# Performance work log

Hardware: AMD Instinct MI355X
Metric: run time of the kernel (lower is better)

Reference implementation:

```python
import jax, jax.numpy as jnp
import numpy as np

B, H, W, D, DFF = 32, 40, 40, 128, 2048
S = H * W  # 1600
BN_EPS = 1e-5


def setup_inputs() -> dict:
    key = jax.random.key(0)
    ks = jax.random.split(key, 8)
    se = jax.random.normal(ks[2], (H, W, H, W), dtype=jnp.float32)
    se = se + jnp.transpose(se, (2, 3, 0, 1))  # symmetric init as in torch code
    wscale = 0.02
    return {
        "tgt": jax.random.normal(ks[0], (B, H, W, D), dtype=jnp.float32),
        "memory": jax.random.normal(ks[1], (B, H, W, D), dtype=jnp.float32),
        "score_embed": se,
        "w1": jax.random.normal(ks[3], (D, D), dtype=jnp.float32) * wscale,
        "b1": jnp.zeros((D,), jnp.float32),
        "g1": jnp.ones((2 * S,), jnp.float32),
        "be1": jnp.zeros((2 * S,), jnp.float32),
        "w2": jax.random.normal(ks[4], (DFF, 2 * S), dtype=jnp.float32) * wscale,
        "b2": jnp.zeros((DFF,), jnp.float32),
        "g2": jnp.ones((DFF,), jnp.float32),
        "be2": jnp.zeros((DFF,), jnp.float32),
        "w3": jax.random.normal(ks[5], (1, DFF), dtype=jnp.float32) * wscale,
        "b3": jnp.zeros((1,), jnp.float32),
        "g3": jnp.ones((1,), jnp.float32),
        "be3": jnp.zeros((1,), jnp.float32),
    }


def _bn_eval(x, gamma, beta):
    # BatchNorm eval mode with running_mean=0, running_var=1 (as initialized)
    return x * (gamma / jnp.sqrt(1.0 + BN_EPS)) + beta


def _l2norm(x):
    # F.normalize(p=2, dim=-1) with eps=1e-12
    return x / jnp.maximum(jnp.linalg.norm(x, axis=-1, keepdims=True), 1e-12)


def reference(tgt, memory, score_embed, w1, b1, g1, be1, w2, b2, g2, be2, w3, b3, g3, be3):
    b, h, w, d = tgt.shape
    s = h * w
    q = _l2norm(tgt.reshape(b, s, d) @ w1.T + b1)   # [B,S,D]
    k = _l2norm(memory.reshape(b, s, d) @ w1.T + b1)
    gate = jax.nn.sigmoid(score_embed.reshape(s, s))  # [S,S]
    attn = jnp.einsum("bsd,btd->bst", q, k) * gate    # [B,S,S]
    m1 = attn.max(axis=1)  # max over dim 1 -> [B,S]
    m2 = attn.max(axis=2)  # max over dim 2 -> [B,S]
    x = jnp.concatenate([m1, m2], axis=1)  # [B,2S]
    x = _bn_eval(x, g1, be1)
    x = x @ w2.T + b2        # [B,DFF]
    x = jax.nn.relu(_bn_eval(x, g2, be2))
    x = x @ w3.T + b3        # [B,1]
    x = _bn_eval(x, g3, be3)
    return x.squeeze(-1)     # [B]
```

## Files before the change

kernel.cpp:

```cpp
#include <hip/hip_runtime.h>
#include <hip/hip_bf16.h>

#define BB 32
#define SS 1600
#define DD 128
#define DFFN 2048
#define S2N 3200
#define RS 136

typedef __attribute__((ext_vector_type(8))) short short8;
typedef __attribute__((ext_vector_type(4))) float floatx4;
typedef unsigned int u32;
typedef unsigned short u16;

__device__ __forceinline__ u32 encf(float f) {
  u32 u = __float_as_uint(f);
  return (u & 0x80000000u) ? ~u : (u | 0x80000000u);
}
__device__ __forceinline__ float decf(u32 e) {
  u32 u = (e & 0x80000000u) ? (e & 0x7fffffffu) : ~e;
  return __uint_as_float(u);
}
__device__ __forceinline__ u16 f2b(float x) {
  u32 u = __float_as_uint(x);
  return (u16)((u + 0x7FFFu + ((u >> 16) & 1u)) >> 16);
}
__device__ __forceinline__ u32 packb2(float lo, float hi) {
  return (u32)f2b(lo) | ((u32)f2b(hi) << 16);
}
__device__ __forceinline__ float sigm(float x) { return 1.f / (1.f + __expf(-x)); }

__global__ __launch_bounds__(256) void k_prep(const float* __restrict__ tgt,
                                              const float* __restrict__ memin,
                                              const float* __restrict__ w1,
                                              const float* __restrict__ b1,
                                              const float* __restrict__ se,
                                              u16* __restrict__ qb, u16* __restrict__ kb,
                                              u16* __restrict__ gT2,
                                              u32* __restrict__ m1u, u32* __restrict__ m2u) {
  __shared__ u16 sA[128 * RS];
  __shared__ u16 sB[128 * RS];
  __shared__ float sq[128];
  int tid = threadIdx.x;
  int lane = tid & 63, wv = tid >> 6;
  int wr = wv >> 1, wc = wv & 1;
  int l15 = lane & 15, lg = lane >> 4;

  if (blockIdx.x >= 800) {
    int bid = blockIdx.x - 800;
    int ii = bid * 256 + tid;
    if (ii < BB * SS) {
      m1u[ii] = 0u;
      m2u[ii] = 0u;
    }
    int r2 = bid >> 2, mi = bid & 3;
    int sy = r2 / 13, tx = r2 - sy * 13;
    int s0 = min(sy * 128, SS - 128);
    int t0 = min(tx * 128, SS - 128);
    int srow = s0 + wr * 64 + mi * 16 + lg * 4;
    u16* tb = gT2 + (size_t)r2 * 16384 + wv * 4096 + lane * 8;
    for (int ni = 0; ni < 4; ++ni) {
      int tcol = t0 + wc * 64 + ni * 16 + l15;
      const float* sp = se + (size_t)srow * SS + tcol;
      ushort4 o;
      o.x = f2b(sigm(sp[0]));
      o.y = f2b(sigm(sp[SS]));
      o.z = f2b(sigm(sp[2 * SS]));
      o.w = f2b(sigm(sp[3 * SS]));
      *(ushort4*)(tb + (mi * 2 + (ni >> 1)) * 512 + (ni & 1) * 4) = o;
    }
    return;
  }

  long row0 = (long)blockIdx.x * 128;
  const float* src;
  u16* dst;
  if (row0 < (long)BB * SS) { src = tgt + row0 * DD; dst = qb + row0 * DD; }
  else { src = memin + (row0 - (long)BB * SS) * DD; dst = kb + (row0 - (long)BB * SS) * DD; }

  for (int p = 0; p < 16; ++p) {
    int r = p * 8 + (tid >> 5);
    int c4 = (tid & 31) * 4;
    float4 v = *(const float4*)(src + r * DD + c4);
    *(u32*)&sA[r * RS + c4] = packb2(v.x, v.y);
    *(u32*)&sA[r * RS + c4 + 2] = packb2(v.z, v.w);
    float4 w = *(const float4*)(w1 + r * DD + c4);
    *(u32*)&sB[r * RS + c4] = packb2(w.x, w.y);
    *(u32*)&sB[r * RS + c4 + 2] = packb2(w.z, w.w);
  }
  if (tid < 128) sq[tid] = 0.f;
  __syncthreads();

  floatx4 acc[4][4];
  for (int mi = 0; mi < 4; ++mi)
    for (int ni = 0; ni < 4; ++ni) acc[mi][ni] = (floatx4){0.f, 0.f, 0.f, 0.f};

  for (int kc = 0; kc < 4; ++kc) {
    int k0 = kc * 32 + lg * 8;
    short8 af[4], bfr[4];
    for (int mi = 0; mi < 4; ++mi) af[mi] = *(const short8*)&sA[(wr * 64 + mi * 16 + l15) * RS + k0];
    for (int ni = 0; ni < 4; ++ni) bfr[ni] = *(const short8*)&sB[(wc * 64 + ni * 16 + l15) * RS + k0];
    for (int mi = 0; mi < 4; ++mi)
      for (int ni = 0; ni < 4; ++ni)
        acc[mi][ni] = __builtin_amdgcn_mfma_f32_16x16x32_bf16(af[mi], bfr[ni], acc[mi][ni], 0, 0, 0);
  }

  float bvals[4];
  for (int ni = 0; ni < 4; ++ni) bvals[ni] = b1[wc * 64 + ni * 16 + l15];
  for (int mi = 0; mi < 4; ++mi)
    for (int r = 0; r < 4; ++r) {
      float s = 0.f;
      for (int ni = 0; ni < 4; ++ni) {
        float v = acc[mi][ni][r] + bvals[ni];
        acc[mi][ni][r] = v;
        s += v * v;
      }
      s += __shfl_xor(s, 1); s += __shfl_xor(s, 2);
      s += __shfl_xor(s, 4); s += __shfl_xor(s, 8);
      if (l15 == 0) atomicAdd(&sq[wr * 64 + mi * 16 + lg * 4 + r], s);
    }
  __syncthreads();

  for (int mi = 0; mi < 4; ++mi)
    for (int r = 0; r < 4; ++r) {
      int row = wr * 64 + mi * 16 + lg * 4 + r;
      float scale = 1.f / fmaxf(sqrtf(sq[row]), 1e-12f);
      for (int ni = 0; ni < 4; ++ni)
        sA[row * RS + wc * 64 + ni * 16 + l15] = f2b(acc[mi][ni][r] * scale);
    }
  __syncthreads();
  for (int p = 0; p < 8; ++p) {
    int r = p * 16 + (tid >> 4);
    int c8 = (tid & 15) * 8;
    *(uint4*)(dst + r * DD + c8) = *(const uint4*)&sA[r * RS + c8];
  }
}

__global__ __launch_bounds__(256, 4) void k_attn(const u16* __restrict__ qb,
                                                 const u16* __restrict__ kb,
                                                 const u16* __restrict__ gT2,
                                                 u32* __restrict__ m1u, u32* __restrict__ m2u) {
  __shared__ u16 sK[128 * RS];
  __shared__ float scmax[2][128];
  __shared__ float srmax[2][128];
  int tid = threadIdx.x;
  int n = blockIdx.x;
  int m = n >> 3;
  int r2 = m >> 2;
  int b = (n & 7) * 4 + (m & 3);
  int sy = r2 / 13, tx = r2 - sy * 13;
  int s0 = min(sy * 128, SS - 128);
  int t0 = min(tx * 128, SS - 128);
  int lane = tid & 63, wv = tid >> 6;
  int wr = wv >> 1, wc = wv & 1;
  int l15 = lane & 15, lg = lane >> 4;
  const size_t base = (size_t)b * SS * DD;
  const u16* qp = qb + base + (size_t)(s0 + wr * 64 + l15) * DD + lg * 8;

  {
    int rr0 = tid >> 4;
    int c8 = (tid & 15) * 8;
    const u16* kp = kb + base + (size_t)(t0 + rr0) * DD + c8;
    u16* sp = &sK[rr0 * RS + c8];
    for (int p = 0; p < 8; ++p)
      *(uint4*)(sp + p * 16 * RS) = *(const uint4*)(kp + (size_t)p * 16 * DD);
  }
  short8 qsA[4], qsB[4];
  for (int mi = 0; mi < 4; ++mi) qsA[mi] = *(const short8*)(qp + mi * 16 * DD);
  __syncthreads();

  floatx4 acc[4][4];
  for (int mi = 0; mi < 4; ++mi)
    for (int ni = 0; ni < 4; ++ni) acc[mi][ni] = (floatx4){0.f, 0.f, 0.f, 0.f};

#define QKSTEP(KC, CUR, NXT, PRE)                                                     \
  {                                                                                   \
    if (PRE)                                                                          \
      for (int mi = 0; mi < 4; ++mi)                                                  \
        NXT[mi] = *(const short8*)(qp + mi * 16 * DD + ((KC) + 1) * 32);              \
    int k0 = (KC)*32 + lg * 8;                                                        \
    short8 bfr[4];                                                                    \
    for (int ni = 0; ni < 4; ++ni)                                                    \
      bfr[ni] = *(const short8*)&sK[(wc * 64 + ni * 16 + l15) * RS + k0];             \
    for (int mi = 0; mi < 4; ++mi)                                                    \
      for (int ni = 0; ni < 4; ++ni)                                                  \
        acc[mi][ni] = __builtin_amdgcn_mfma_f32_16x16x32_bf16(CUR[mi], bfr[ni],       \
                                                              acc[mi][ni], 0, 0, 0);  \
  }
  QKSTEP(0, qsA, qsB, 1)
  QKSTEP(1, qsB, qsA, 1)
  QKSTEP(2, qsA, qsB, 1)
  QKSTEP(3, qsB, qsA, 0)
#undef QKSTEP

  uint4 g4[8];
  {
    const u16* gbase = gT2 + (size_t)r2 * 16384 + wv * 4096 + lane * 8;
    for (int p = 0; p < 8; ++p) g4[p] = *(const uint4*)(gbase + p * 512);
  }

  float rmax[4][4];
  for (int mi = 0; mi < 4; ++mi)
    for (int r = 0; r < 4; ++r) rmax[mi][r] = -1e30f;
  float cmax[4];
  for (int ni = 0; ni < 4; ++ni) cmax[ni] = -1e30f;

  for (int mi = 0; mi < 4; ++mi)
    for (int ni = 0; ni < 4; ++ni) {
      uint4 pg = g4[mi * 2 + (ni >> 1)];
      u32 lo = (ni & 1) ? pg.z : pg.x;
      u32 hi = (ni & 1) ? pg.w : pg.y;
      float v0 = acc[mi][ni][0] * __uint_as_float(lo << 16);
      float v1 = acc[mi][ni][1] * __uint_as_float(lo & 0xffff0000u);
      float v2 = acc[mi][ni][2] * __uint_as_float(hi << 16);
      float v3 = acc[mi][ni][3] * __uint_as_float(hi & 0xffff0000u);
      rmax[mi][0] = fmaxf(rmax[mi][0], v0);
      rmax[mi][1] = fmaxf(rmax[mi][1], v1);
      rmax[mi][2] = fmaxf(rmax[mi][2], v2);
      rmax[mi][3] = fmaxf(rmax[mi][3], v3);
      cmax[ni] = fmaxf(cmax[ni], fmaxf(fmaxf(v0, v1), fmaxf(v2, v3)));
    }

  for (int ni = 0; ni < 4; ++ni) {
    cmax[ni] = fmaxf(cmax[ni], __shfl_xor(cmax[ni], 16));
    cmax[ni] = fmaxf(cmax[ni], __shfl_xor(cmax[ni], 32));
  }
  if (lane < 16)
    for (int ni = 0; ni < 4; ++ni) scmax[wr][wc * 64 + ni * 16 + lane] = cmax[ni];

  for (int mi = 0; mi < 4; ++mi)
    for (int r = 0; r < 4; ++r) {
      float v = rmax[mi][r];
      v = fmaxf(v, __shfl_xor(v, 1));
      v = fmaxf(v, __shfl_xor(v, 2));
      v = fmaxf(v, __shfl_xor(v, 4));
      v = fmaxf(v, __shfl_xor(v, 8));
      if (l15 == 0) srmax[wc][wr * 64 + mi * 16 + lg * 4 + r] = v;
    }
  __syncthreads();

  if (tid < 128) {
    float v = fmaxf(scmax[0][tid], scmax[1][tid]);
    atomicMax(&m1u[b * SS + t0 + tid], encf(v));
  } else {
    int i2 = tid - 128;
    float v = fmaxf(srmax[0][i2], srmax[1][i2]);
    atomicMax(&m2u[b * SS + s0 + i2], encf(v));
  }
}

__global__ __launch_bounds__(256) void k_gemm2(const u32* __restrict__ m1u,
                                               const u32* __restrict__ m2u,
                                               const float* __restrict__ g1,
                                               const float* __restrict__ be1,
                                               const float* __restrict__ w2,
                                               float* __restrict__ hacc) {
  int tid = threadIdx.x;
  int lane = tid & 63, wv = tid >> 6;
  int f0 = blockIdx.x * 32 + wv * 8;
  int cs = blockIdx.y;
  int cr0 = cs * 200;
  const u32* msrc = (cs < 8) ? m1u : m2u;
  int mcol0 = cr0 - ((cs < 8) ? 0 : SS);
  int c_sub = lane & 15, bq = lane >> 4;
  const float bnc = rsqrtf(1.f + 1e-5f);
  float acc[8][8];
  for (int a = 0; a < 8; ++a)
    for (int c = 0; c < 8; ++c) acc[a][c] = 0.f;
  const float4 z4 = {0.f, 0.f, 0.f, 0.f};
  for (int it = 0; it < 4; ++it) {
    int coff = it * 64 + c_sub * 4;
    bool ok = coff < 200;
    int cg = cr0 + coff;
    float4 w4[8], x4[8];
    float4 gv = ok ? *(const float4*)(g1 + cg) : z4;
    float4 bv = ok ? *(const float4*)(be1 + cg) : z4;
    gv.x *= bnc; gv.y *= bnc; gv.z *= bnc; gv.w *= bnc;
    for (int jf = 0; jf < 8; ++jf)
      w4[jf] = ok ? *(const float4*)(w2 + (size_t)(f0 + jf) * S2N + cg) : z4;
    for (int j = 0; j < 8; ++j) {
      if (ok) {
        uint4 e = *(const uint4*)(msrc + (size_t)(bq * 8 + j) * SS + mcol0 + coff);
        x4[j].x = decf(e.x) * gv.x + bv.x;
        x4[j].y = decf(e.y) * gv.y + bv.y;
        x4[j].z = decf(e.z) * gv.z + bv.z;
        x4[j].w = decf(e.w) * gv.w + bv.w;
      } else {
        x4[j] = z4;
      }
    }
    for (int jf = 0; jf < 8; ++jf)
      for (int j = 0; j < 8; ++j) {
        float a = acc[jf][j];
        a = fmaf(w4[jf].x, x4[j].x, a);
        a = fmaf(w4[jf].y, x4[j].y, a);
        a = fmaf(w4[jf].z, x4[j].z, a);
        a = fmaf(w4[jf].w, x4[j].w, a);
        acc[jf][j] = a;
      }
  }
  for (int jf = 0; jf < 8; ++jf)
    for (int j = 0; j < 8; ++j) {
      float v = acc[jf][j];
      v += __shfl_xor(v, 1); v += __shfl_xor(v, 2);
      v += __shfl_xor(v, 4); v += __shfl_xor(v, 8);
      acc[jf][j] = v;
    }
  if ((lane & 15) == 0) {
    for (int jf = 0; jf < 8; ++jf)
      for (int j = 0; j < 8; ++j) {
        int b = bq * 8 + j;
        hacc[((size_t)cs * BB + b) * DFFN + f0 + jf] = acc[jf][j];
      }
  }
}

__global__ __launch_bounds__(512) void k_final(const float* __restrict__ hacc,
                                               const float* __restrict__ b2,
                                               const float* __restrict__ g2,
                                               const float* __restrict__ be2,
                                               const float* __restrict__ w3,
                                               const float* __restrict__ b3,
                                               const float* __restrict__ g3,
                                               const float* __restrict__ be3,
                                               float* __restrict__ out) {
  __shared__ float wsum[8];
  int b = blockIdx.x;
  int tid = threadIdx.x;
  float bnc = rsqrtf(1.f + 1e-5f);
  int f4i = tid;
  float4 s4 = *(const float4*)(b2 + f4i * 4);
  for (int cs = 0; cs < 16; ++cs) {
    float4 h = *(const float4*)(hacc + ((size_t)cs * BB + b) * DFFN + f4i * 4);
    s4.x += h.x; s4.y += h.y; s4.z += h.z; s4.w += h.w;
  }
  float4 gv = *(const float4*)(g2 + f4i * 4);
  float4 bv = *(const float4*)(be2 + f4i * 4);
  float4 w4 = *(const float4*)(w3 + f4i * 4);
  float part = 0.f;
  part += fmaxf(s4.x * (gv.x * bnc) + bv.x, 0.f) * w4.x;
  part += fmaxf(s4.y * (gv.y * bnc) + bv.y, 0.f) * w4.y;
  part += fmaxf(s4.z * (gv.z * bnc) + bv.z, 0.f) * w4.z;
  part += fmaxf(s4.w * (gv.w * bnc) + bv.w, 0.f) * w4.w;
  for (int m = 1; m < 64; m <<= 1) part += __shfl_xor(part, m);
  if ((tid & 63) == 0) wsum[tid >> 6] = part;
  __syncthreads();
  if (tid == 0) {
    float tot = b3[0];
    for (int wq = 0; wq < 8; ++wq) tot += wsum[wq];
    out[b] = tot * (g3[0] * bnc) + be3[0];
  }
}

extern "C" void kernel_launch(void* const* d_in, const int* in_sizes, int n_in,
                              void* d_out, int out_size, void* d_ws, size_t ws_size,
                              hipStream_t stream) {
  const float* tgt = (const float*)d_in[0];
  const float* memin = (const float*)d_in[1];
  const float* se = (const float*)d_in[2];
  const float* w1 = (const float*)d_in[3];
  const float* b1 = (const float*)d_in[4];
  const float* g1 = (const float*)d_in[5];
  const float* be1 = (const float*)d_in[6];
  const float* w2 = (const float*)d_in[7];
  const float* b2 = (const float*)d_in[8];
  const float* g2 = (const float*)d_in[9];
  const float* be2 = (const float*)d_in[10];
  const float* w3 = (const float*)d_in[11];
  const float* b3 = (const float*)d_in[12];
  const float* g3 = (const float*)d_in[13];
  const float* be3 = (const float*)d_in[14];
  float* out = (float*)d_out;

  char* ws = (char*)d_ws;
  const size_t OFF_GT = 0;
  const size_t OFF_QB = 5537792;
  const size_t OFF_KB = OFF_QB + 13107200;
  const size_t OFF_M1 = OFF_KB + 13107200;
  const size_t OFF_M2 = OFF_M1 + 204800;
  const size_t OFF_HA = OFF_M2 + 204800;
  const size_t NEEDED = OFF_HA + 4194304;
  if (ws_size < NEEDED) return;

  u16* gT2 = (u16*)(ws + OFF_GT);
  u16* qb = (u16*)(ws + OFF_QB);
  u16* kb = (u16*)(ws + OFF_KB);
  u32* m1u = (u32*)(ws + OFF_M1);
  u32* m2u = (u32*)(ws + OFF_M2);
  float* hacc = (float*)(ws + OFF_HA);

  k_prep<<<1476, 256, 0, stream>>>(tgt, memin, w1, b1, se, qb, kb, gT2, m1u, m2u);
  k_attn<<<5408, 256, 0, stream>>>(qb, kb, gT2, m1u, m2u);
  k_gemm2<<<dim3(64, 16), 256, 0, stream>>>(m1u, m2u, g1, be1, w2, hacc);
  k_final<<<32, 512, 0, stream>>>(hacc, b2, g2, be2, w3, b3, g3, be3, out);
}
```

Measured before the change: 135.6 us.

## Split projection prep into bf16 conversion kernel and register-fed projection GEMM

Replaces the fused prep kernel with two kernels. A streaming kernel converts tgt, memory and w1 to bf16, computes the sigmoid gate tiles and zeroes the max buffers. A separate projection kernel then reads the bf16 activations and weights straight from global memory into registers, double-buffering the A fragments, and normalizes rows in place. This removes LDS staging and the per-block re-conversion of w1, at the cost of an extra launch and an extra round trip of the bf16 activations through memory. The hacc workspace is moved to overlap the gate buffer.

```diff
diff --git a/kernel.cpp b/kernel.cpp
--- a/kernel.cpp
+++ b/kernel.cpp
@@ -30,80 +30,111 @@
 }
 __device__ __forceinline__ float sigm(float x) { return 1.f / (1.f + __expf(-x)); }
 
-__global__ __launch_bounds__(256) void k_prep(const float* __restrict__ tgt,
+__global__ __launch_bounds__(256) void k_conv(const float* __restrict__ tgt,
                                               const float* __restrict__ memin,
                                               const float* __restrict__ w1,
-                                              const float* __restrict__ b1,
                                               const float* __restrict__ se,
                                               u16* __restrict__ qb, u16* __restrict__ kb,
+                                              u16* __restrict__ w1b,
                                               u16* __restrict__ gT2,
                                               u32* __restrict__ m1u, u32* __restrict__ m2u) {
-  __shared__ u16 sA[128 * RS];
-  __shared__ u16 sB[128 * RS];
+  int tid = threadIdx.x;
+  int bid = blockIdx.x;
+  if (bid < 1600) {
+    const float4* src4;
+    uint2* dst2;
+    int cb;
+    if (bid < 800) { src4 = (const float4*)tgt; dst2 = (uint2*)qb; cb = bid; }
+    else { src4 = (const float4*)memin; dst2 = (uint2*)kb; cb = bid - 800; }
+    int base = cb * 2048 + tid;
+    float4 v[8];
+    for (int j = 0; j < 8; ++j) v[j] = src4[base + j * 256];
+    for (int j = 0; j < 8; ++j) {
+      uint2 o;
+      o.x = packb2(v[j].x, v[j].y);
+      o.y = packb2(v[j].z, v[j].w);
+      dst2[base + j * 256] = o;
+    }
+    return;
+  }
+  int gbid = bid - 1600;
+  int ii = gbid * 256 + tid;
+  if (ii < 4096) {
+    float4 w = ((const float4*)w1)[ii];
+    ushort4 o;
+    o.x = f2b(w.x); o.y = f2b(w.y); o.z = f2b(w.z); o.w = f2b(w.w);
+    ((ushort4*)w1b)[ii] = o;
+  }
+  if (ii < BB * SS) {
+    m1u[ii] = 0u;
+    m2u[ii] = 0u;
+  }
+  int lane = tid & 63, wv = tid >> 6;
+  int wr = wv >> 1, wc = wv & 1;
+  int l15 = lane & 15, lg = lane >> 4;
+  int r2 = gbid >> 2, mi = gbid & 3;
+  int sy = r2 / 13, tx = r2 - sy * 13;
+  int s0 = min(sy * 128, SS - 128);
+  int t0 = min(tx * 128, SS - 128);
+  int srow = s0 + wr * 64 + mi * 16 + lg * 4;
+  u16* tb = gT2 + (size_t)r2 * 16384 + wv * 4096 + lane * 8;
+  for (int ni = 0; ni < 4; ++ni) {
+    int tcol = t0 + wc * 64 + ni * 16 + l15;
+    const float* sp = se + (size_t)srow * SS + tcol;
+    ushort4 o;
+    o.x = f2b(sigm(sp[0]));
+    o.y = f2b(sigm(sp[SS]));
+    o.z = f2b(sigm(sp[2 * SS]));
+    o.w = f2b(sigm(sp[3 * SS]));
+    *(ushort4*)(tb + (mi * 2 + (ni >> 1)) * 512 + (ni & 1) * 4) = o;
+  }
+}
+
+__global__ __launch_bounds__(256, 3) void k_proj(u16* __restrict__ qb, u16* __restrict__ kb,
+                                                 const u16* __restrict__ w1b,
+                                                 const float* __restrict__ b1) {
+  __shared__ u16 sO[128 * RS];
   __shared__ float sq[128];
   int tid = threadIdx.x;
   int lane = tid & 63, wv = tid >> 6;
   int wr = wv >> 1, wc = wv & 1;
   int l15 = lane & 15, lg = lane >> 4;
-
-  if (blockIdx.x >= 800) {
-    int bid = blockIdx.x - 800;
-    int ii = bid * 256 + tid;
-    if (ii < BB * SS) {
-      m1u[ii] = 0u;
-      m2u[ii] = 0u;
-    }
-    int r2 = bid >> 2, mi = bid & 3;
-    int sy = r2 / 13, tx = r2 - sy * 13;
-    int s0 = min(sy * 128, SS - 128);
-    int t0 = min(tx * 128, SS - 128);
-    int srow = s0 + wr * 64 + mi * 16 + lg * 4;
-    u16* tb = gT2 + (size_t)r2 * 16384 + wv * 4096 + lane * 8;
-    for (int ni = 0; ni < 4; ++ni) {
-      int tcol = t0 + wc * 64 + ni * 16 + l15;
-      const float* sp = se + (size_t)srow * SS + tcol;
-      ushort4 o;
-      o.x = f2b(sigm(sp[0]));
-      o.y = f2b(sigm(sp[SS]));
-      o.z = f2b(sigm(sp[2 * SS]));
-      o.w = f2b(sigm(sp[3 * SS]));
-      *(ushort4*)(tb + (mi * 2 + (ni >> 1)) * 512 + (ni & 1) * 4) = o;
-    }
-    return;
-  }
-
-  long row0 = (long)blockIdx.x * 128;
-  const float* src;
-  u16* dst;
-  if (row0 < (long)BB * SS) { src = tgt + row0 * DD; dst = qb + row0 * DD; }
-  else { src = memin + (row0 - (long)BB * SS) * DD; dst = kb + (row0 - (long)BB * SS) * DD; }
-
-  for (int p = 0; p < 16; ++p) {
-    int r = p * 8 + (tid >> 5);
-    int c4 = (tid & 31) * 4;
-    float4 v = *(const float4*)(src + r * DD + c4);
-    *(u32*)&sA[r * RS + c4] = packb2(v.x, v.y);
-    *(u32*)&sA[r * RS + c4 + 2] = packb2(v.z, v.w);
-    float4 w = *(const float4*)(w1 + r * DD + c4);
-    *(u32*)&sB[r * RS + c4] = packb2(w.x, w.y);
-    *(u32*)&sB[r * RS + c4 + 2] = packb2(w.z, w.w);
-  }
+  int bidm = blockIdx.x;
+  u16* x = (bidm < 400) ? qb : kb;
+  long row0 = (long)(bidm % 400) * 128;
+  u16* xp = x + (size_t)row0 * DD;
+  const u16* qp = xp + (size_t)(wr * 64 + l15) * DD + lg * 8;
+
   if (tid < 128) sq[tid] = 0.f;
-  __syncthreads();
+
+  short8 qsA[4], qsB[4];
+  for (int mi = 0; mi < 4; ++mi) qsA[mi] = *(const short8*)(qp + mi * 16 * DD);
 
   floatx4 acc[4][4];
   for (int mi = 0; mi < 4; ++mi)
     for (int ni = 0; ni < 4; ++ni) acc[mi][ni] = (floatx4){0.f, 0.f, 0.f, 0.f};
 
-  for (int kc = 0; kc < 4; ++kc) {
-    int k0 = kc * 32 + lg * 8;
-    short8 af[4], bfr[4];
-    for (int mi = 0; mi < 4; ++mi) af[mi] = *(const short8*)&sA[(wr * 64 + mi * 16 + l15) * RS + k0];
-    for (int ni = 0; ni < 4; ++ni) bfr[ni] = *(const short8*)&sB[(wc * 64 + ni * 16 + l15) * RS + k0];
-    for (int mi = 0; mi < 4; ++mi)
-      for (int ni = 0; ni < 4; ++ni)
-        acc[mi][ni] = __builtin_amdgcn_mfma_f32_16x16x32_bf16(af[mi], bfr[ni], acc[mi][ni], 0, 0, 0);
-  }
+#define PSTEP(KC, CUR, NXT, PRE)                                                      \
+  {                                                                                   \
+    if (PRE)                                                                          \
+      for (int mi = 0; mi < 4; ++mi)                                                  \
+        NXT[mi] = *(const short8*)(qp + mi * 16 * DD + ((KC) + 1) * 32);              \
+    int k0 = (KC)*32 + lg * 8;                                                        \
+    short8 bfr[4];                                                                    \
+    for (int ni = 0; ni < 4; ++ni)                                                    \
+      bfr[ni] = *(const short8*)(w1b + (size_t)(wc * 64 + ni * 16 + l15) * DD + k0);  \
+    for (int mi = 0; mi < 4; ++mi)                                                    \
+      for (int ni = 0; ni < 4; ++ni)                                                  \
+        acc[mi][ni] = __builtin_amdgcn_mfma_f32_16x16x32_bf16(CUR[mi], bfr[ni],       \
+                                                              acc[mi][ni], 0, 0, 0);  \
+  }
+  PSTEP(0, qsA, qsB, 1)
+  PSTEP(1, qsB, qsA, 1)
+  PSTEP(2, qsA, qsB, 1)
+  PSTEP(3, qsB, qsA, 0)
+#undef PSTEP
+
+  __syncthreads();
 
   float bvals[4];
   for (int ni = 0; ni < 4; ++ni) bvals[ni] = b1[wc * 64 + ni * 16 + l15];
@@ -126,13 +157,13 @@
       int row = wr * 64 + mi * 16 + lg * 4 + r;
       float scale = 1.f / fmaxf(sqrtf(sq[row]), 1e-12f);
       for (int ni = 0; ni < 4; ++ni)
-        sA[row * RS + wc * 64 + ni * 16 + l15] = f2b(acc[mi][ni][r] * scale);
+        sO[row * RS + wc * 64 + ni * 16 + l15] = f2b(acc[mi][ni][r] * scale);
     }
   __syncthreads();
   for (int p = 0; p < 8; ++p) {
     int r = p * 16 + (tid >> 4);
     int c8 = (tid & 15) * 8;
-    *(uint4*)(dst + r * DD + c8) = *(const uint4*)&sA[r * RS + c8];
+    *(uint4*)(xp + (size_t)r * DD + c8) = *(const uint4*)&sO[r * RS + c8];
   }
 }
 
@@ -378,8 +409,9 @@
   const size_t OFF_KB = OFF_QB + 13107200;
   const size_t OFF_M1 = OFF_KB + 13107200;
   const size_t OFF_M2 = OFF_M1 + 204800;
-  const size_t OFF_HA = OFF_M2 + 204800;
-  const size_t NEEDED = OFF_HA + 4194304;
+  const size_t OFF_W1B = OFF_M2 + 204800;
+  const size_t NEEDED = OFF_W1B + 32768;
+  const size_t OFF_HA = 0;
   if (ws_size < NEEDED) return;
 
   u16* gT2 = (u16*)(ws + OFF_GT);
@@ -387,9 +419,11 @@
   u16* kb = (u16*)(ws + OFF_KB);
   u32* m1u = (u32*)(ws + OFF_M1);
   u32* m2u = (u32*)(ws + OFF_M2);
+  u16* w1b = (u16*)(ws + OFF_W1B);
   float* hacc = (float*)(ws + OFF_HA);
 
-  k_prep<<<1476, 256, 0, stream>>>(tgt, memin, w1, b1, se, qb, kb, gT2, m1u, m2u);
+  k_conv<<<2276, 256, 0, stream>>>(tgt, memin, w1, se, qb, kb, w1b, gT2, m1u, m2u);
+  k_proj<<<800, 256, 0, stream>>>(qb, kb, w1b, b1);
   k_attn<<<5408, 256, 0, stream>>>(qb, kb, gT2, m1u, m2u);
   k_gemm2<<<dim3(64, 16), 256, 0, stream>>>(m1u, m2u, g1, be1, w2, hacc);
   k_final<<<32, 512, 0, stream>>>(hacc, b2, g2, be2, w3, b3, g3, be3, out);
```

New measurement: 151.2 us. +11.5%, slower.
